# Kernel tuning notes

Measured on AMD Instinct MI355X. Metric: run time of the kernel, lower is better.

Reference implementation:

```python
import jax, jax.numpy as jnp
import numpy as np

D_MODEL = 512
BINS = 64


def setup_inputs() -> dict:
    key = jax.random.key(0)
    ks = jax.random.split(key, 5)
    x = jax.random.normal(ks[0], (1, 512, D_MODEL), dtype=jnp.float32)
    # torch Linear(2d, d): weight [d, 2d]; store transposed [2d, d] for x @ W
    s1 = 1.0 / np.sqrt(2 * D_MODEL)
    W1 = jax.random.uniform(ks[1], (2 * D_MODEL, D_MODEL), jnp.float32, -s1, s1)
    b1 = jax.random.uniform(ks[2], (D_MODEL,), jnp.float32, -s1, s1)
    s2 = 1.0 / np.sqrt(D_MODEL)
    W2 = jax.random.uniform(ks[3], (D_MODEL, BINS), jnp.float32, -s2, s2)
    b2 = jax.random.uniform(ks[4], (BINS,), jnp.float32, -s2, s2)
    return {"x": x, "W1": W1, "b1": b1, "W2": W2, "b2": b2}


def reference(x, W1, b1, W2, b2):
    # pair = cat([xi, xj], -1); Linear(cat) == xi @ W1[:d] + xj @ W1[d:]
    # This factorization is exact and avoids materializing the [B,N,N,2d] tensor.
    d = x.shape[-1]
    hi = jnp.einsum('bnd,de->bne', x, W1[:d])      # [B, N, d]
    hj = jnp.einsum('bnd,de->bne', x, W1[d:])      # [B, N, d]
    h = hi[:, :, None, :] + hj[:, None, :, :] + b1  # [B, N, N, d]
    h = jax.nn.gelu(h, approximate=False)           # torch nn.GELU default is exact
    return jnp.einsum('bijd,de->bije', h, W2) + b2  # [B, N, N, bins]
```

## Files before the change

### kernel.cpp

```cpp
#include <hip/hip_runtime.h>
#include <hip/hip_fp16.h>

#define D 512
#define NTOK 512
#define BINS 64

typedef float v4f __attribute__((ext_vector_type(4)));
typedef int v4i __attribute__((ext_vector_type(4)));
typedef short short8 __attribute__((ext_vector_type(8)));
typedef _Float16 h8 __attribute__((ext_vector_type(8)));
typedef _Float16 h4 __attribute__((ext_vector_type(4)));

__device__ __forceinline__ __half2 gelu2(__half2 x) {
    __half2 s = __hmul2(x, x);
    __half2 q = __hmul2(x, __hfma2(s, __float2half2_rn(-0.1029437f),
                                      __float2half2_rn(-2.3022082f)));
    __half2 e = h2exp2(q);
    __half2 r = h2rcp(__hadd2(e, __float2half2_rn(1.0f)));
    return __hmul2(x, r);
}

__device__ __forceinline__ __half2 bc_h2(int v) { return __builtin_bit_cast(__half2, v); }
__device__ __forceinline__ int bc_i(__half2 v) { return __builtin_bit_cast(int, v); }

__global__ __launch_bounds__(256) void k_proj(const float* __restrict__ x,
                                              const float* __restrict__ W1,
                                              const float* __restrict__ b1,
                                              const float* __restrict__ W2,
                                              __half* __restrict__ hi,
                                              __half* __restrict__ hj,
                                              short8* __restrict__ Bp) {
    const int b = blockIdx.x;
    if (b >= 512) {
        const int tid = (b - 512) * 256 + threadIdx.x;
        const int ll = tid & 63;
        const int nt = (tid >> 6) & 3;
        const int kt = tid >> 8;
        const int colp = nt * 16 + (ll & 15);
        const int krow = kt * 32 + (ll >> 4) * 8;
        short8 v;
#pragma unroll
        for (int u = 0; u < 8; ++u) {
            _Float16 hv = (_Float16)W2[(size_t)(krow + u) * BINS + colp];
            v[u] = __builtin_bit_cast(short, hv);
        }
        Bp[tid] = v;
        return;
    }
    const int rb = b >> 4, cg = b & 15;
    __shared__ __align__(16) float xs[16][516];
    const float* xsrc = x + (size_t)rb * 16 * D;
#pragma unroll
    for (int i = 0; i < 8; ++i) {
        int e = (threadIdx.x + 256 * i) * 4;
        *(v4f*)&xs[e >> 9][e & 511] = *(const v4f*)(xsrc + e);
    }
    __syncthreads();

    const int l = threadIdx.x & 63;
    const int w = threadIdx.x >> 6;
    const int row = w * 4 + (l >> 4);
    const int col4 = (l & 15) * 4;
    const int half = cg >> 3;
    const int e0 = (cg & 7) * 64 + col4;
    const float* Wp = W1 + (size_t)half * (D * D) + e0;
    v4f acc = {0.f, 0.f, 0.f, 0.f};
    if (half == 0) acc = *(const v4f*)(b1 + e0);
#pragma unroll 4
    for (int k = 0; k < D; k += 4) {
        v4f xa = *(const v4f*)&xs[row][k];
        v4f w0 = *(const v4f*)(Wp + (size_t)(k + 0) * D);
        v4f w1 = *(const v4f*)(Wp + (size_t)(k + 1) * D);
        v4f w2 = *(const v4f*)(Wp + (size_t)(k + 2) * D);
        v4f w3 = *(const v4f*)(Wp + (size_t)(k + 3) * D);
        acc += xa.x * w0;
        acc += xa.y * w1;
        acc += xa.z * w2;
        acc += xa.w * w3;
    }
    h4 o;
    o[0] = (_Float16)acc.x; o[1] = (_Float16)acc.y;
    o[2] = (_Float16)acc.z; o[3] = (_Float16)acc.w;
    __half* dst = (half ? hj : hi) + (size_t)(rb * 16 + row) * D + e0;
    *(h4*)dst = o;
}

__global__ __launch_bounds__(256) void k_main(const __half* __restrict__ hi,
                                              const __half* __restrict__ hj,
                                              const v4i* __restrict__ Bp,
                                              const float* __restrict__ b2,
                                              float* __restrict__ out) {
    const int l = threadIdx.x & 63;
    const int w = threadIdx.x >> 6;
    const int c = l & 15;
    const int q = l >> 4;
    const int ib = (blockIdx.x >> 5) * 16;
    const int j0 = (blockIdx.x & 31) * 16;

    __shared__ __align__(16) short hic[16][72];
    __shared__ __align__(16) short hjc[16][72];

    const int t = threadIdx.x;
    const int lr = (t & 127) >> 3;
    const int lc = (t & 7) * 8;
    const __half* gsrc = (t < 128 ? hi + (size_t)(ib + lr) * D
                                  : hj + (size_t)(j0 + lr) * D) + lc;
    short* ldst = (t < 128 ? &hic[lr][lc] : &hjc[lr][lc]);

    v4f acc[4][4] = {};
    v4i pf = *(const v4i*)gsrc;

    for (int chunk = 0; chunk < 8; ++chunk) {
        *(v4i*)ldst = pf;
        __syncthreads();
        if (chunk < 7) pf = *(const v4i*)(gsrc + (chunk + 1) * 64);
        const int kt4 = chunk * 8;
#pragma unroll
        for (int h = 0; h < 2; ++h) {
            const int ko = h * 32 + q * 8;
            v4i hjraw = *(const v4i*)&hjc[c][ko];
            __half2 j0h = bc_h2(hjraw.x), j1h = bc_h2(hjraw.y);
            __half2 j2h = bc_h2(hjraw.z), j3h = bc_h2(hjraw.w);
            v4i bfr[4];
#pragma unroll
            for (int nt = 0; nt < 4; ++nt)
                bfr[nt] = Bp[(kt4 + h * 4 + nt) * 64 + l];
#pragma unroll
            for (int p = 0; p < 4; ++p) {
                v4i ar = *(const v4i*)&hic[w * 4 + p][ko];
                __half2 g0 = gelu2(__hadd2(bc_h2(ar.x), j0h));
                __half2 g1 = gelu2(__hadd2(bc_h2(ar.y), j1h));
                __half2 g2 = gelu2(__hadd2(bc_h2(ar.z), j2h));
                __half2 g3 = gelu2(__hadd2(bc_h2(ar.w), j3h));
                v4i ai = {bc_i(g0), bc_i(g1), bc_i(g2), bc_i(g3)};
                h8 af = __builtin_bit_cast(h8, ai);
#pragma unroll
                for (int nt = 0; nt < 4; ++nt)
                    acc[p][nt] = __builtin_amdgcn_mfma_f32_16x16x32_f16(
                        af, __builtin_bit_cast(h8, bfr[nt]), acc[p][nt], 0, 0, 0);
            }
        }
        __syncthreads();
    }

    const int i0 = ib + w * 4;
#pragma unroll
    for (int p = 0; p < 4; ++p) {
        const size_t rowbase = ((size_t)(i0 + p) * NTOK + j0 + q * 4) * BINS;
#pragma unroll
        for (int nt = 0; nt < 4; ++nt) {
            const float bb = b2[nt * 16 + c];
            float* op = out + rowbase + nt * 16 + c;
#pragma unroll
            for (int rr = 0; rr < 4; ++rr)
                op[(size_t)rr * BINS] = acc[p][nt][rr] + bb;
        }
    }
}

extern "C" void kernel_launch(void* const* d_in, const int* in_sizes, int n_in,
                              void* d_out, int out_size, void* d_ws, size_t ws_size,
                              hipStream_t stream) {
    const float* x  = (const float*)d_in[0];
    const float* W1 = (const float*)d_in[1];
    const float* b1 = (const float*)d_in[2];
    const float* W2 = (const float*)d_in[3];
    const float* b2 = (const float*)d_in[4];
    float* out = (float*)d_out;

    char* ws = (char*)d_ws;
    __half* hi = (__half*)ws;
    __half* hj = (__half*)(ws + (512u << 10));
    short8* Bp = (short8*)(ws + (1u << 20));

    k_proj<<<528, 256, 0, stream>>>(x, W1, b1, W2, hi, hj, Bp);
    k_main<<<1024, 256, 0, stream>>>(hi, hj, (const v4i*)Bp, b2, out);
}
```

Before: 151.1 us.

## Compute input projection with fp16 MFMA after packing x and W1 into fragment layout

The FP32 FMA projection kernel is replaced by two kernels. The first converts x, W1 and W2 to fp16 and packs them in MFMA fragment order. The second runs the 512x1024x512 projection with 16x16x32 f16 MFMA and adds b1 for the first half. This moves the projection onto matrix cores, at the cost of an extra launch, an extra workspace round trip, and fp16 rounding of the projection inputs.

Result: faster. 129.1 us (-14.6%).

```diff
diff --git a/kernel.cpp b/kernel.cpp
--- a/kernel.cpp
+++ b/kernel.cpp
@@ -23,16 +23,48 @@
 __device__ __forceinline__ __half2 bc_h2(int v) { return __builtin_bit_cast(__half2, v); }
 __device__ __forceinline__ int bc_i(__half2 v) { return __builtin_bit_cast(int, v); }
 
-__global__ __launch_bounds__(256) void k_proj(const float* __restrict__ x,
+__device__ __forceinline__ v4i pack8(v4f a, v4f b) {
+    h8 o;
+    o[0] = (_Float16)a.x; o[1] = (_Float16)a.y; o[2] = (_Float16)a.z; o[3] = (_Float16)a.w;
+    o[4] = (_Float16)b.x; o[5] = (_Float16)b.y; o[6] = (_Float16)b.z; o[7] = (_Float16)b.w;
+    return __builtin_bit_cast(v4i, o);
+}
+
+__global__ __launch_bounds__(256) void k_pack(const float* __restrict__ x,
                                               const float* __restrict__ W1,
-                                              const float* __restrict__ b1,
                                               const float* __restrict__ W2,
-                                              __half* __restrict__ hi,
-                                              __half* __restrict__ hj,
+                                              v4i* __restrict__ Ap,
+                                              v4i* __restrict__ Wp,
                                               short8* __restrict__ Bp) {
     const int b = blockIdx.x;
-    if (b >= 512) {
-        const int tid = (b - 512) * 256 + threadIdx.x;
+    const int t = threadIdx.x;
+    if (b < 32) {
+        const int rb = b;
+#pragma unroll
+        for (int u = 0; u < 4; ++u) {
+            const int e = t + 256 * u;
+            const int l = e & 63, ks = e >> 6;
+            const float* src = x + (size_t)(rb * 16 + (l & 15)) * D + ks * 32 + (l >> 4) * 8;
+            v4f a = *(const v4f*)src;
+            v4f c = *(const v4f*)(src + 4);
+            Ap[(size_t)(rb * 16 + ks) * 64 + l] = pack8(a, c);
+        }
+    } else if (b < 96) {
+        const int nb = b - 32;
+#pragma unroll
+        for (int u = 0; u < 4; ++u) {
+            const int e = t + 256 * u;
+            const int l = e & 63, ks = e >> 6;
+            const int ng = nb * 16 + (l & 15);
+            const float* src = W1 + (size_t)((ng >> 9) * D + ks * 32 + (l >> 4) * 8) * D
+                                  + (ng & 511);
+            h8 o;
+#pragma unroll
+            for (int j = 0; j < 8; ++j) o[j] = (_Float16)src[(size_t)j * D];
+            Wp[(size_t)(nb * 16 + ks) * 64 + l] = __builtin_bit_cast(v4i, o);
+        }
+    } else {
+        const int tid = (b - 96) * 256 + t;
         const int ll = tid & 63;
         const int nt = (tid >> 6) & 3;
         const int kt = tid >> 8;
@@ -45,44 +77,49 @@
             v[u] = __builtin_bit_cast(short, hv);
         }
         Bp[tid] = v;
-        return;
-    }
-    const int rb = b >> 4, cg = b & 15;
-    __shared__ __align__(16) float xs[16][516];
-    const float* xsrc = x + (size_t)rb * 16 * D;
-#pragma unroll
-    for (int i = 0; i < 8; ++i) {
-        int e = (threadIdx.x + 256 * i) * 4;
-        *(v4f*)&xs[e >> 9][e & 511] = *(const v4f*)(xsrc + e);
-    }
-    __syncthreads();
-
+    }
+}
+
+__global__ __launch_bounds__(256) void k_gemm(const v4i* __restrict__ Ap,
+                                              const v4i* __restrict__ Wp,
+                                              const float* __restrict__ b1,
+                                              _Float16* __restrict__ hi,
+                                              _Float16* __restrict__ hj) {
     const int l = threadIdx.x & 63;
     const int w = threadIdx.x >> 6;
-    const int row = w * 4 + (l >> 4);
-    const int col4 = (l & 15) * 4;
-    const int half = cg >> 3;
-    const int e0 = (cg & 7) * 64 + col4;
-    const float* Wp = W1 + (size_t)half * (D * D) + e0;
-    v4f acc = {0.f, 0.f, 0.f, 0.f};
-    if (half == 0) acc = *(const v4f*)(b1 + e0);
+    const int c = l & 15;
+    const int q = l >> 4;
+    const int mb = blockIdx.x >> 4;
+    const int cb = blockIdx.x & 15;
+    const int nb = cb * 4 + w;
+
+    const v4i* ap0 = Ap + (size_t)(mb * 2 + 0) * 16 * 64 + l;
+    const v4i* ap1 = Ap + (size_t)(mb * 2 + 1) * 16 * 64 + l;
+    const v4i* wp  = Wp + (size_t)nb * 16 * 64 + l;
+
+    v4f acc0 = {0.f, 0.f, 0.f, 0.f};
+    v4f acc1 = {0.f, 0.f, 0.f, 0.f};
 #pragma unroll 4
-    for (int k = 0; k < D; k += 4) {
-        v4f xa = *(const v4f*)&xs[row][k];
-        v4f w0 = *(const v4f*)(Wp + (size_t)(k + 0) * D);
-        v4f w1 = *(const v4f*)(Wp + (size_t)(k + 1) * D);
-        v4f w2 = *(const v4f*)(Wp + (size_t)(k + 2) * D);
-        v4f w3 = *(const v4f*)(Wp + (size_t)(k + 3) * D);
-        acc += xa.x * w0;
-        acc += xa.y * w1;
-        acc += xa.z * w2;
-        acc += xa.w * w3;
-    }
-    h4 o;
-    o[0] = (_Float16)acc.x; o[1] = (_Float16)acc.y;
-    o[2] = (_Float16)acc.z; o[3] = (_Float16)acc.w;
-    __half* dst = (half ? hj : hi) + (size_t)(rb * 16 + row) * D + e0;
-    *(h4*)dst = o;
+    for (int ks = 0; ks < 16; ++ks) {
+        v4i a0 = ap0[ks * 64];
+        v4i a1 = ap1[ks * 64];
+        v4i bb = wp[ks * 64];
+        h8 bf = __builtin_bit_cast(h8, bb);
+        acc0 = __builtin_amdgcn_mfma_f32_16x16x32_f16(__builtin_bit_cast(h8, a0), bf, acc0, 0, 0, 0);
+        acc1 = __builtin_amdgcn_mfma_f32_16x16x32_f16(__builtin_bit_cast(h8, a1), bf, acc1, 0, 0, 0);
+    }
+
+    const int ng = nb * 16 + c;
+    const float b1v = (ng < D) ? b1[ng] : 0.0f;
+    _Float16* dst = (ng < D ? hi : hj) + (ng & 511);
+#pragma unroll
+    for (int mf = 0; mf < 2; ++mf) {
+        v4f acc = mf ? acc1 : acc0;
+        const int row0 = mb * 32 + mf * 16 + q * 4;
+#pragma unroll
+        for (int r = 0; r < 4; ++r)
+            dst[(size_t)(row0 + r) * D] = (_Float16)(acc[r] + b1v);
+    }
 }
 
 __global__ __launch_bounds__(256) void k_main(const __half* __restrict__ hi,
@@ -172,7 +209,10 @@
     __half* hi = (__half*)ws;
     __half* hj = (__half*)(ws + (512u << 10));
     short8* Bp = (short8*)(ws + (1u << 20));
-
-    k_proj<<<528, 256, 0, stream>>>(x, W1, b1, W2, hi, hj, Bp);
+    v4i*    Ap = (v4i*)(ws + (1u << 20) + (64u << 10));
+    v4i*    Wp = (v4i*)(ws + (1u << 20) + (64u << 10) + (512u << 10));
+
+    k_pack<<<112, 256, 0, stream>>>(x, W1, W2, Ap, Wp, Bp);
+    k_gemm<<<256, 256, 0, stream>>>(Ap, Wp, b1, (_Float16*)hi, (_Float16*)hj);
     k_main<<<1024, 256, 0, stream>>>(hi, hj, (const v4i*)Bp, b2, out);
 }
```
